# Optimization experiments

Measured on AMD Instinct MI355X. Metric: run time of the kernel, lower is better.

## Reference

```python
import jax, jax.numpy as jnp
import numpy as np

B, N, DIM = 8, 512, 512
HEADS, HD = 8, 64          # head_dim = dim // num_heads
E_ATT = 24                 # num_attn_experts, top-k = HEADS
E_FFD, K_FFD = 16, 2       # num_ffd_experts, top-k = ffd_heads
HID = 1024                 # int(dim*mlp_ratio) // ffd_heads = 2048 // 2
TASKS = 9
SWITCH_W, Z_W = 0.01, 0.001
SCALE = HD ** -0.5


def layer_norm(x, g, b, eps=1e-5):
    m = x.mean(-1, keepdims=True)
    v = ((x - m) ** 2).mean(-1, keepdims=True)
    return (x - m) * jax.lax.rsqrt(v + eps) * g + b


def top_k_gating(xf, w_gate, k, n_experts):
    # xf: [T, C], w_gate: [C, E]  (eval mode: no noise)
    logits = xf @ w_gate                                      # [T, E]
    probs = jax.nn.softmax(logits, axis=-1)
    vals, idx = jax.lax.top_k(probs, k)                       # [T, k]
    denom = jax.lax.stop_gradient(vals.sum(-1, keepdims=True) + 1e-6)
    gates = vals / denom                                      # renormalized top-k gates
    one_hot = jax.nn.one_hot(idx, n_experts, dtype=probs.dtype)  # [T, k, E]
    freqs = jax.lax.stop_gradient(one_hot.sum((0, 1)))        # tokens per expert [E]
    p_sum = probs.sum(0)
    switch = n_experts * jnp.sum((p_sum / p_sum.sum()) * (freqs / freqs.sum()))
    z = jnp.mean(jax.nn.logsumexp(logits, axis=-1) ** 2)
    loss = SWITCH_W * switch + Z_W * z
    return gates, one_hot, loss


def _forward(x, task_bh, norm1_g, norm1_b, gate_att, wq, wo_att, kv_w, kv_b,
             norm2_g, norm2_b, gate_mlp, wi, bi, wo_mlp, bo):
    Bs, Ns, C = x.shape
    T = Bs * Ns
    # ---- MoE task attention (MoA-style: experts produce query heads) ----
    x1 = layer_norm(x, norm1_g, norm1_b).reshape(T, C)
    gates, oh, loss1 = top_k_gating(x1, gate_att[task_bh], HEADS, E_ATT)
    # map: per-slot expert query projection (not gate-weighted)
    q_all = jnp.einsum('tc,ech->teh', x1, wq)                 # [T, E, hd]
    q = jnp.einsum('teh,tke->tkh', q_all, oh)                 # [T, H, hd]
    q = q.reshape(Bs, Ns, HEADS, HD)
    kv = x1 @ kv_w + kv_b                                     # shared single-head k,v
    k_, v_ = jnp.split(kv.reshape(Bs, Ns, 2 * HD), 2, axis=-1)
    attn = jnp.einsum('bihd,bjd->bhij', q, k_) * SCALE
    attn = jax.nn.softmax(attn, axis=-1)
    o = jnp.einsum('bhij,bjd->bihd', attn, v_).reshape(T, HEADS, HD)
    # reduce: gate-weighted per-expert output projection
    comb = jnp.einsum('tkd,tk,tke->ted', o, gates, oh)        # [T, E, hd]
    y = jnp.einsum('ted,edc->tc', comb, wo_att).reshape(Bs, Ns, C)
    x = x + y
    # ---- MoE task MLP ----
    x2 = layer_norm(x, norm2_g, norm2_b).reshape(T, C)
    gates2, oh2, loss2 = top_k_gating(x2, gate_mlp[task_bh], K_FFD, E_FFD)
    g_dense = jnp.einsum('tk,tke->te', gates2, oh2)           # sparse gates densified [T,E]
    h = jax.nn.gelu(jnp.einsum('tc,ech->teh', x2, wi) + bi, approximate=False)
    y2 = jnp.einsum('teh,te,ehc->tc', h, g_dense, wo_mlp) + g_dense @ bo
    x = x + y2.reshape(Bs, Ns, C)
    return x, loss1 + loss2


def setup_inputs() -> dict:
    key = jax.random.key(0)
    ks = jax.random.split(key, 8)
    s = 0.02
    return {
        'x': jax.random.normal(ks[0], (B, N, DIM), jnp.float32),
        'task_bh': 3,
        'norm1_g': jnp.ones((DIM,), jnp.float32),
        'norm1_b': jnp.zeros((DIM,), jnp.float32),
        'gate_att': jax.random.normal(ks[1], (TASKS, DIM, E_ATT), jnp.float32) * s,
        'wq': jax.random.normal(ks[2], (E_ATT, DIM, HD), jnp.float32) * s,
        'wo_att': jax.random.normal(ks[3], (E_ATT, HD, DIM), jnp.float32) * s,
        'kv_w': jax.random.normal(ks[4], (DIM, 2 * HD), jnp.float32) * s,
        'kv_b': jnp.zeros((2 * HD,), jnp.float32),
        'norm2_g': jnp.ones((DIM,), jnp.float32),
        'norm2_b': jnp.zeros((DIM,), jnp.float32),
        'gate_mlp': jax.random.normal(ks[5], (TASKS, DIM, E_FFD), jnp.float32) * s,
        'wi': jax.random.normal(ks[6], (E_FFD, DIM, HID), jnp.float32) * s,
        'bi': jnp.zeros((E_FFD, HID), jnp.float32),
        'wo_mlp': jax.random.normal(ks[7], (E_FFD, HID, DIM), jnp.float32) * s,
        'bo': jnp.zeros((E_FFD, DIM), jnp.float32),
    }


def reference(x, task_bh, norm1_g, norm1_b, gate_att, wq, wo_att, kv_w, kv_b,
              norm2_g, norm2_b, gate_mlp, wi, bi, wo_mlp, bo):
    return _forward(x, task_bh, norm1_g, norm1_b, gate_att, wq, wo_att, kv_w, kv_b,
                    norm2_g, norm2_b, gate_mlp, wi, bi, wo_mlp, bo)
```

## Files before the change

### kernel.cpp

```cpp
#include <hip/hip_runtime.h>
#include <math.h>

namespace {

constexpr int T   = 4096;
constexpr int C   = 512;
constexpr int NB  = 8;
constexpr int NS  = 512;
constexpr int HD  = 64;
constexpr int KA  = 8;
constexpr int EA  = 24;
constexpr int EF  = 16;
constexpr int KF  = 2;
constexpr int HID = 1024;

typedef __attribute__((ext_vector_type(8))) short bf16x8;
typedef __attribute__((ext_vector_type(4))) float f32x4;

__device__ inline unsigned short f2bf(float f) {
  unsigned u = __float_as_uint(f);
  return (unsigned short)((u + 0x7FFFu + ((u >> 16) & 1u)) >> 16);
}
__device__ inline float bf2f(unsigned short u) {
  return __uint_as_float((unsigned)u << 16);
}

template <int E, int TS>
__device__ inline bool tile_from_counts(const int* counts, int tile, int& e_out, int& t0_out) {
  int e = 0;
  for (; e < E; e++) {
    int nt = (counts[e] + TS - 1) / TS;
    if (tile < nt) break;
    tile -= nt;
  }
  e_out = e; t0_out = tile * TS;
  return e < E;
}

template <int E, int K>
__global__ __launch_bounds__(512) void ln_gate_kernel(
    const float* __restrict__ in, const float* __restrict__ g,
    const float* __restrict__ b, const float* __restrict__ gate_all,
    const int* __restrict__ task, unsigned short* __restrict__ outb,
    float* __restrict__ probs, float* __restrict__ lse_out,
    float* __restrict__ gates, int* __restrict__ idxs) {
  constexpr int TPB = 16;
  constexpr int XSS = 516;
  constexpr int WSS = 516;
  int tid = threadIdx.x, lane = tid & 63, wv = tid >> 6;
  int tb = blockIdx.x * TPB;
  __shared__ float xs[TPB][XSS];
  __shared__ float lg[TPB][E];
  __shared__ __align__(16) float Wt[E][WSS];
  const float* W = gate_all + (size_t)task[0] * C * E;
  for (int i = tid; i < C * E; i += 512) {
    int c = i / E, e = i - c * E;
    Wt[e][c] = W[i];
  }
  int c0 = lane * 8;
  const float4 g0 = *(const float4*)&g[c0], g1 = *(const float4*)&g[c0 + 4];
  const float4 b0 = *(const float4*)&b[c0], b1 = *(const float4*)&b[c0 + 4];
  #pragma unroll
  for (int i = 0; i < 2; i++) {
    int tt = wv * 2 + i;
    int t = tb + tt;
    const float* row = in + (size_t)t * C + c0;
    const float4 v0 = *(const float4*)&row[0];
    const float4 v1 = *(const float4*)&row[4];
    float s = (v0.x + v0.y) + (v0.z + v0.w) + (v1.x + v1.y) + (v1.z + v1.w);
    #pragma unroll
    for (int m = 1; m < 64; m <<= 1) s += __shfl_xor(s, m);
    float mean = s * (1.f / C);
    float d[8] = {v0.x - mean, v0.y - mean, v0.z - mean, v0.w - mean,
                  v1.x - mean, v1.y - mean, v1.z - mean, v1.w - mean};
    float vv = 0.f;
    #pragma unroll
    for (int j = 0; j < 8; j++) vv += d[j] * d[j];
    #pragma unroll
    for (int m = 1; m < 64; m <<= 1) vv += __shfl_xor(vv, m);
    float r = rsqrtf(vv * (1.f / C) + 1e-5f);
    float o[8];
    o[0] = d[0] * r * g0.x + b0.x; o[1] = d[1] * r * g0.y + b0.y;
    o[2] = d[2] * r * g0.z + b0.z; o[3] = d[3] * r * g0.w + b0.w;
    o[4] = d[4] * r * g1.x + b1.x; o[5] = d[5] * r * g1.y + b1.y;
    o[6] = d[6] * r * g1.z + b1.z; o[7] = d[7] * r * g1.w + b1.w;
    *(ushort4*)&outb[(size_t)t * C + c0] =
        make_ushort4(f2bf(o[0]), f2bf(o[1]), f2bf(o[2]), f2bf(o[3]));
    *(ushort4*)&outb[(size_t)t * C + c0 + 4] =
        make_ushort4(f2bf(o[4]), f2bf(o[5]), f2bf(o[6]), f2bf(o[7]));
    #pragma unroll
    for (int j = 0; j < 8; j++) xs[tt][c0 + j] = o[j];
  }
  __syncthreads();
  if (tid < TPB * E) {
    int e = tid % E, tt = tid / E;
    float a0 = 0.f, a1 = 0.f, a2 = 0.f, a3 = 0.f;
    float a4 = 0.f, a5 = 0.f, a6 = 0.f, a7 = 0.f;
    #pragma unroll 4
    for (int c = 0; c < C; c += 8) {
      const float4 xv0 = *(const float4*)&xs[tt][c];
      const float4 xv1 = *(const float4*)&xs[tt][c + 4];
      const float4 wv0 = *(const float4*)&Wt[e][c];
      const float4 wv1 = *(const float4*)&Wt[e][c + 4];
      a0 += xv0.x * wv0.x; a1 += xv0.y * wv0.y;
      a2 += xv0.z * wv0.z; a3 += xv0.w * wv0.w;
      a4 += xv1.x * wv1.x; a5 += xv1.y * wv1.y;
      a6 += xv1.z * wv1.z; a7 += xv1.w * wv1.w;
    }
    lg[tt][e] = ((a0 + a1) + (a2 + a3)) + ((a4 + a5) + (a6 + a7));
  }
  __syncthreads();
  #pragma unroll
  for (int i = 0; i < 2; i++) {
    int tt = wv * 2 + i;
    int t = tb + tt;
    float lgv = (lane < E) ? lg[tt][lane] : -3.0e38f;
    float mx = lgv;
    #pragma unroll
    for (int m = 1; m < 64; m <<= 1) mx = fmaxf(mx, __shfl_xor(mx, m));
    float pe = (lane < E) ? expf(lgv - mx) : 0.f;
    float sum = pe;
    #pragma unroll
    for (int m = 1; m < 64; m <<= 1) sum += __shfl_xor(sum, m);
    float inv = 1.f / sum;
    float prob = pe * inv;
    if (lane < E) probs[(size_t)t * E + lane] = prob;
    if (lane == 0) lse_out[t] = mx + logf(sum);
    float pv = (lane < E) ? prob : -1.f;
    float gsum = 0.f, myv = 0.f; int myi = 0;
    for (int k = 0; k < K; k++) {
      float bv = pv; int bi_ = lane;
      #pragma unroll
      for (int m = 1; m < 64; m <<= 1) {
        float ov = __shfl_xor(bv, m); int oi = __shfl_xor(bi_, m);
        if (ov > bv || (ov == bv && oi < bi_)) { bv = ov; bi_ = oi; }
      }
      gsum += bv;
      if (lane == k) { myv = bv; myi = bi_; }
      if (lane == bi_) pv = -1.f;
    }
    if (lane < K) {
      float ginv = 1.f / (gsum + 1e-6f);
      gates[(size_t)t * K + lane] = myv * ginv;
      idxs[(size_t)t * K + lane]  = myi;
    }
  }
}

template <int E>
__global__ __launch_bounds__(512) void bucket_kernel(const int* __restrict__ idx, int nslots,
                                                     int stride, int* counts, int* bucket) {
  __shared__ int lcount[E];
  __shared__ int lbase[E];
  int tid = threadIdx.x;
  if (tid < E) lcount[tid] = 0;
  __syncthreads();
  int s = blockIdx.x * 512 + tid;
  int e = 0, lpos = 0;
  bool valid = (s < nslots);
  if (valid) {
    e = idx[s];
    lpos = atomicAdd(&lcount[e], 1);
  }
  __syncthreads();
  if (tid < E) lbase[tid] = lcount[tid] ? atomicAdd(&counts[tid], lcount[tid]) : 0;
  __syncthreads();
  if (valid) bucket[(size_t)e * stride + lbase[e] + lpos] = s;
}

__global__ __launch_bounds__(256) void tcvt_all(
    const float* __restrict__ wq, const float* __restrict__ wo_a,
    const float* __restrict__ wi, const float* __restrict__ wo_m,
    const float* __restrict__ kvw,
    unsigned short* __restrict__ wqt, unsigned short* __restrict__ woat,
    unsigned short* __restrict__ wit, unsigned short* __restrict__ womt,
    unsigned short* __restrict__ kvwt) {
  int bid = blockIdx.x;
  const float* src; unsigned short* dst; int K, N, nx, rem;
  if (bid < 768)        { src = wq;   dst = wqt;  K = 512;  N = 64;   nx = 2;  rem = bid; }
  else if (bid < 1536)  { src = wo_a; dst = woat; K = 64;   N = 512;  nx = 16; rem = bid - 768; }
  else if (bid < 9728)  { src = wi;   dst = wit;  K = 512;  N = 1024; nx = 32; rem = bid - 1536; }
  else if (bid < 17920) { src = wo_m; dst = womt; K = 1024; N = 512;  nx = 16; rem = bid - 9728; }
  else                  { src = kvw;  dst = kvwt; K = 512;  N = 128;  nx = 4;  rem = bid - 17920; }
  int per = nx * (K / 32);
  int e = rem / per, r2 = rem % per;
  int kt = (r2 / nx) * 32, nt = (r2 % nx) * 32;
  __shared__ float tile[32][33];
  int tid = threadIdx.x;
  const float* S = src + (size_t)e * K * N;
  for (int i = tid; i < 32 * 32; i += 256) {
    int r = i >> 5, c = i & 31;
    tile[r][c] = S[(size_t)(kt + r) * N + nt + c];
  }
  __syncthreads();
  unsigned short* D = dst + (size_t)e * K * N;
  for (int i = tid; i < 32 * 8; i += 256) {
    int n = i >> 3, k4 = (i & 7) * 4;
    ushort4 v;
    v.x = f2bf(tile[k4 + 0][n]); v.y = f2bf(tile[k4 + 1][n]);
    v.z = f2bf(tile[k4 + 2][n]); v.w = f2bf(tile[k4 + 3][n]);
    *(ushort4*)&D[(size_t)(nt + n) * K + kt + k4] = v;
  }
}

__global__ __launch_bounds__(256) void qgemm_mfma(
    const unsigned short* __restrict__ xb, const unsigned short* __restrict__ wqt,
    const int* __restrict__ bucket, const int* __restrict__ counts,
    unsigned short* __restrict__ qb) {
  __shared__ int se, st0;
  int tid = threadIdx.x;
  if (tid == 0) {
    int e, t0;
    bool ok = tile_from_counts<EA, 64>(counts, blockIdx.y, e, t0);
    se = ok ? e : -1; st0 = t0;
  }
  __syncthreads();
  if (se < 0) return;
  int e = se, t0 = st0;
  int cnt = counts[e];
  __shared__ int slots[64];
  __shared__ __align__(16) unsigned short Xb[64][72];
  __shared__ __align__(16) unsigned short Wb[64][72];
  if (tid < 64) {
    int ii = t0 + tid;
    slots[tid] = (ii < cnt) ? bucket[(size_t)e * (T * KA) + ii] : -1;
  }
  __syncthreads();
  int lane = tid & 63, w = tid >> 6;
  int lr = lane & 15, lk = (lane >> 4) * 8, rowq = (lane >> 4) * 4;
  f32x4 acc[4] = {};
  for (int kc = 0; kc < C; kc += 64) {
    __syncthreads();
    #pragma unroll
    for (int it = 0; it < 2; ++it) {
      int i = it * 256 + tid;
      int r = i >> 3, c8 = (i & 7) * 8;
      int s = slots[r];
      uint4 v = make_uint4(0u, 0u, 0u, 0u);
      if (s >= 0) v = *(const uint4*)&xb[(size_t)(s >> 3) * C + kc + c8];
      *(uint4*)&Xb[r][c8] = v;
    }
    #pragma unroll
    for (int it = 0; it < 2; ++it) {
      int i = it * 256 + tid;
      int r = i >> 3, c8 = (i & 7) * 8;
      *(uint4*)&Wb[r][c8] = *(const uint4*)&wqt[((size_t)e * HD + r) * C + kc + c8];
    }
    __syncthreads();
    #pragma unroll
    for (int kk = 0; kk < 64; kk += 32) {
      bf16x8 a = *(const bf16x8*)&Wb[w * 16 + lr][kk + lk];
      #pragma unroll
      for (int mf = 0; mf < 4; mf++) {
        bf16x8 b = *(const bf16x8*)&Xb[mf * 16 + lr][kk + lk];
        acc[mf] = __builtin_amdgcn_mfma_f32_16x16x32_bf16(a, b, acc[mf], 0, 0, 0);
      }
    }
  }
  #pragma unroll
  for (int mf = 0; mf < 4; mf++) {
    int s = slots[mf * 16 + lr];
    if (s < 0) continue;
    ushort4 v = make_ushort4(f2bf(0.125f * acc[mf][0]), f2bf(0.125f * acc[mf][1]),
                             f2bf(0.125f * acc[mf][2]), f2bf(0.125f * acc[mf][3]));
    *(ushort4*)&qb[(size_t)s * HD + w * 16 + rowq] = v;
  }
}

__global__ __launch_bounds__(256) void kv_mfma(
    const unsigned short* __restrict__ xb, const unsigned short* __restrict__ kvwt,
    const float* __restrict__ kvb, unsigned short* __restrict__ Kb,
    unsigned short* __restrict__ Vt) {
  int t0 = blockIdx.x * 16;
  int tid = threadIdx.x;
  __shared__ __align__(16) unsigned short Xs[16][72];
  __shared__ __align__(16) unsigned short Ws[128][72];
  int lane = tid & 63, w = tid >> 6;
  int lr = lane & 15, lk = (lane >> 4) * 8, rowq = (lane >> 4) * 4;
  f32x4 acc[2] = {};
  for (int kc = 0; kc < C; kc += 64) {
    __syncthreads();
    if (tid < 128) {
      int r = tid >> 3, c8 = (tid & 7) * 8;
      *(uint4*)&Xs[r][c8] = *(const uint4*)&xb[(size_t)(t0 + r) * C + kc + c8];
    }
    #pragma unroll
    for (int it = 0; it < 4; ++it) {
      int i = it * 256 + tid;
      int r = i >> 3, c8 = (i & 7) * 8;
      *(uint4*)&Ws[r][c8] = *(const uint4*)&kvwt[(size_t)r * C + kc + c8];
    }
    __syncthreads();
    #pragma unroll
    for (int kk = 0; kk < 64; kk += 32) {
      bf16x8 xf = *(const bf16x8*)&Xs[lr][kk + lk];
      #pragma unroll
      for (int cf = 0; cf < 2; cf++) {
        bf16x8 wf = *(const bf16x8*)&Ws[w * 32 + cf * 16 + lr][kk + lk];
        acc[cf] = __builtin_amdgcn_mfma_f32_16x16x32_bf16(wf, xf, acc[cf], 0, 0, 0);
      }
    }
  }
  int t = t0 + lr;
  int bb = t >> 9, n = t & (NS - 1);
  #pragma unroll
  for (int cf = 0; cf < 2; cf++) {
    #pragma unroll
    for (int r2 = 0; r2 < 4; r2++) {
      int c = w * 32 + cf * 16 + rowq + r2;
      float v = acc[cf][r2] + kvb[c];
      if (c < HD) Kb[(size_t)t * HD + c] = f2bf(v);
      else        Vt[((size_t)bb * HD + (c - HD)) * NS + n] = f2bf(v);
    }
  }
}

__global__ __launch_bounds__(256) void attn_mfma(
    const unsigned short* __restrict__ qb, const unsigned short* __restrict__ Kb,
    const unsigned short* __restrict__ Vt, unsigned short* __restrict__ ob) {
  int qt = blockIdx.x, h = blockIdx.y, b = blockIdx.z;
  int tid = threadIdx.x;
  __shared__ __align__(16) unsigned short Qs[64][72];
  __shared__ __align__(16) unsigned short Ks[64][72];
  __shared__ __align__(16) unsigned short Vs[64][72];
  __shared__ __align__(16) unsigned short Ps[64][72];
  int i0 = qt * 64;
  #pragma unroll
  for (int it = 0; it < 2; ++it) {
    int i = it * 256 + tid;
    int r = i >> 3, c8 = (i & 7) * 8;
    *(uint4*)&Qs[r][c8] = *(const uint4*)&qb[(((size_t)(b * NS + i0 + r)) * KA + h) * HD + c8];
  }
  int lane = tid & 63, w = tid >> 6;
  int lr = lane & 15, lk = (lane >> 4) * 8, rowq = (lane >> 4) * 4;
  f32x4 acc_o[4] = {};
  float m_run = -3.0e38f, l_run = 0.f;
  for (int jt = 0; jt < NS / 64; ++jt) {
    __syncthreads();
    #pragma unroll
    for (int it = 0; it < 2; ++it) {
      int i = it * 256 + tid;
      int r = i >> 3, c8 = (i & 7) * 8;
      *(uint4*)&Ks[r][c8] = *(const uint4*)&Kb[((size_t)(b * NS + jt * 64 + r)) * HD + c8];
      *(uint4*)&Vs[r][c8] = *(const uint4*)&Vt[((size_t)b * HD + r) * NS + jt * 64 + c8];
    }
    __syncthreads();
    f32x4 acc_s[4] = {};
    #pragma unroll
    for (int kk = 0; kk < 64; kk += 32) {
      bf16x8 qf = *(const bf16x8*)&Qs[w * 16 + lr][kk + lk];
      #pragma unroll
      for (int kf = 0; kf < 4; kf++) {
        bf16x8 kr = *(const bf16x8*)&Ks[kf * 16 + lr][kk + lk];
        acc_s[kf] = __builtin_amdgcn_mfma_f32_16x16x32_bf16(kr, qf, acc_s[kf], 0, 0, 0);
      }
    }
    float pmax = acc_s[0][0];
    #pragma unroll
    for (int kf = 0; kf < 4; kf++)
      #pragma unroll
      for (int r = 0; r < 4; r++) pmax = fmaxf(pmax, acc_s[kf][r]);
    pmax = fmaxf(pmax, __shfl_xor(pmax, 16));
    pmax = fmaxf(pmax, __shfl_xor(pmax, 32));
    float m_new = fmaxf(m_run, pmax);
    float scl = expf(m_run - m_new);
    float rs = 0.f;
    #pragma unroll
    for (int kf = 0; kf < 4; kf++)
      #pragma unroll
      for (int r = 0; r < 4; r++) {
        float pv = expf(acc_s[kf][r] - m_new);
        rs += pv;
        Ps[w * 16 + lr][kf * 16 + rowq + r] = f2bf(pv);
      }
    rs += __shfl_xor(rs, 16);
    rs += __shfl_xor(rs, 32);
    l_run = l_run * scl + rs;
    m_run = m_new;
    __syncthreads();
    #pragma unroll
    for (int df = 0; df < 4; df++) {
      acc_o[df][0] *= scl; acc_o[df][1] *= scl;
      acc_o[df][2] *= scl; acc_o[df][3] *= scl;
    }
    #pragma unroll
    for (int kk = 0; kk < 64; kk += 32) {
      bf16x8 pf = *(const bf16x8*)&Ps[w * 16 + lr][kk + lk];
      #pragma unroll
      for (int df = 0; df < 4; df++) {
        bf16x8 vf = *(const bf16x8*)&Vs[df * 16 + lr][kk + lk];
        acc_o[df] = __builtin_amdgcn_mfma_f32_16x16x32_bf16(vf, pf, acc_o[df], 0, 0, 0);
      }
    }
  }
  float inv = 1.f / l_run;
  int token = b * NS + i0 + w * 16 + lr;
  #pragma unroll
  for (int df = 0; df < 4; df++) {
    ushort4 v = make_ushort4(f2bf(acc_o[df][0] * inv), f2bf(acc_o[df][1] * inv),
                             f2bf(acc_o[df][2] * inv), f2bf(acc_o[df][3] * inv));
    *(ushort4*)&ob[((size_t)token * KA + h) * HD + df * 16 + rowq] = v;
  }
}

__global__ __launch_bounds__(256) void oproj_mfma(
    const unsigned short* __restrict__ ob, const unsigned short* __restrict__ wot,
    const float* __restrict__ gates, const int* __restrict__ bucket,
    const int* __restrict__ counts, unsigned short* __restrict__ y_slot) {
  __shared__ int se, st0;
  int tid = threadIdx.x;
  if (tid == 0) {
    int e, t0;
    bool ok = tile_from_counts<EA, 128>(counts, blockIdx.y, e, t0);
    se = ok ? e : -1; st0 = t0;
  }
  __syncthreads();
  if (se < 0) return;
  int e = se, t0 = st0;
  int c0 = blockIdx.x * 128;
  int cnt = counts[e];
  __shared__ int slots[128];
  __shared__ float gs[128];
  __shared__ __align__(16) unsigned short Xb[128][72];
  __shared__ __align__(16) unsigned short Wb[128][72];
  if (tid < 128) {
    int ii = t0 + tid;
    int s = (ii < cnt) ? bucket[(size_t)e * (T * KA) + ii] : -1;
    slots[tid] = s;
    gs[tid] = (s >= 0) ? gates[s] : 0.f;
  }
  __syncthreads();
  #pragma unroll
  for (int it = 0; it < 4; ++it) {
    int i = it * 256 + tid;
    int r = i >> 3, c8 = (i & 7) * 8;
    int s = slots[r];
    uint4 vo = make_uint4(0u, 0u, 0u, 0u);
    if (s >= 0) {
      float g = gs[r];
      uint4 u = *(const uint4*)&ob[(size_t)s * HD + c8];
      const unsigned short* us = (const unsigned short*)&u;
      unsigned short* vs = (unsigned short*)&vo;
      #pragma unroll
      for (int k = 0; k < 8; k++) vs[k] = f2bf(g * bf2f(us[k]));
    }
    *(uint4*)&Xb[r][c8] = vo;
  }
  #pragma unroll
  for (int it = 0; it < 4; ++it) {
    int i = it * 256 + tid;
    int r = i >> 3, c8 = (i & 7) * 8;
    *(uint4*)&Wb[r][c8] = *(const uint4*)&wot[((size_t)e * C + c0 + r) * HD + c8];
  }
  __syncthreads();
  int lane = tid & 63, wid = tid >> 6;
  int wr = wid & 1, wc = wid >> 1;
  int lr = lane & 15, lk = (lane >> 4) * 8, rowq = (lane >> 4) * 4;
  f32x4 acc[4][4] = {};
  #pragma unroll
  for (int kk = 0; kk < 64; kk += 32) {
    bf16x8 a[4], b[4];
    #pragma unroll
    for (int nf = 0; nf < 4; nf++) a[nf] = *(const bf16x8*)&Wb[wc * 64 + nf * 16 + lr][kk + lk];
    #pragma unroll
    for (int mf = 0; mf < 4; mf++) b[mf] = *(const bf16x8*)&Xb[wr * 64 + mf * 16 + lr][kk + lk];
    #pragma unroll
    for (int nf = 0; nf < 4; nf++)
      #pragma unroll
      for (int mf = 0; mf < 4; mf++)
        acc[nf][mf] = __builtin_amdgcn_mfma_f32_16x16x32_bf16(a[nf], b[mf], acc[nf][mf], 0, 0, 0);
  }
  #pragma unroll
  for (int mf = 0; mf < 4; mf++) {
    int si = wr * 64 + mf * 16 + lr;
    int s = slots[si];
    if (s < 0) continue;
    size_t base = (size_t)s * C + c0 + wc * 64;
    #pragma unroll
    for (int nf = 0; nf < 4; nf++) {
      ushort4 v = make_ushort4(f2bf(acc[nf][mf][0]), f2bf(acc[nf][mf][1]),
                               f2bf(acc[nf][mf][2]), f2bf(acc[nf][mf][3]));
      *(ushort4*)&y_slot[base + nf * 16 + rowq] = v;
    }
  }
}

__global__ void combine_kernel(const float* __restrict__ x, const unsigned short* __restrict__ ys,
                               float* __restrict__ out) {
  int t = blockIdx.x, tid = threadIdx.x;
  int c = tid * 2;
  float s0 = 0.f, s1 = 0.f;
  #pragma unroll
  for (int k = 0; k < KA; k++) {
    unsigned u = *(const unsigned*)&ys[((size_t)t * KA + k) * C + c];
    s0 += bf2f((unsigned short)(u & 0xFFFF));
    s1 += bf2f((unsigned short)(u >> 16));
  }
  out[(size_t)t * C + c]     = x[(size_t)t * C + c] + s0;
  out[(size_t)t * C + c + 1] = x[(size_t)t * C + c + 1] + s1;
}

__global__ __launch_bounds__(256) void mlp1_mfma(
    const unsigned short* __restrict__ xb, const unsigned short* __restrict__ wit,
    const float* __restrict__ bi, const int* __restrict__ bucket,
    const int* __restrict__ counts, unsigned short* __restrict__ h) {
  __shared__ int se, st0;
  int tid = threadIdx.x;
  if (tid == 0) {
    int e, t0;
    bool ok = tile_from_counts<EF, 64>(counts, blockIdx.y, e, t0);
    se = ok ? e : -1; st0 = t0;
  }
  __syncthreads();
  if (se < 0) return;
  int e = se, t0 = st0;
  int j0 = blockIdx.x * 64;
  int cnt = counts[e];
  __shared__ int slots[64];
  __shared__ __align__(16) unsigned short Xb[64][72];
  __shared__ __align__(16) unsigned short Wb[64][72];
  if (tid < 64) {
    int ii = t0 + tid;
    slots[tid] = (ii < cnt) ? bucket[(size_t)e * (T * KF) + ii] : -1;
  }
  __syncthreads();
  int lane = tid & 63, w = tid >> 6;
  int lr = lane & 15, lk = (lane >> 4) * 8, rowq = (lane >> 4) * 4;
  f32x4 acc[4] = {};
  for (int kc = 0; kc < C; kc += 64) {
    __syncthreads();
    #pragma unroll
    for (int it = 0; it < 2; ++it) {
      int i = it * 256 + tid;
      int r = i >> 3, c8 = (i & 7) * 8;
      int s = slots[r];
      uint4 v = make_uint4(0u, 0u, 0u, 0u);
      if (s >= 0) v = *(const uint4*)&xb[(size_t)(s >> 1) * C + kc + c8];
      *(uint4*)&Xb[r][c8] = v;
    }
    #pragma unroll
    for (int it = 0; it < 2; ++it) {
      int i = it * 256 + tid;
      int r = i >> 3, c8 = (i & 7) * 8;
      *(uint4*)&Wb[r][c8] = *(const uint4*)&wit[((size_t)e * HID + j0 + r) * C + kc + c8];
    }
    __syncthreads();
    #pragma unroll
    for (int kk = 0; kk < 64; kk += 32) {
      bf16x8 a = *(const bf16x8*)&Wb[w * 16 + lr][kk + lk];
      #pragma unroll
      for (int mf = 0; mf < 4; mf++) {
        bf16x8 b = *(const bf16x8*)&Xb[mf * 16 + lr][kk + lk];
        acc[mf] = __builtin_amdgcn_mfma_f32_16x16x32_bf16(a, b, acc[mf], 0, 0, 0);
      }
    }
  }
  #pragma unroll
  for (int mf = 0; mf < 4; mf++) {
    int s = slots[mf * 16 + lr];
    if (s < 0) continue;
    int j = j0 + w * 16 + rowq;
    const float4 b4 = *(const float4*)&bi[(size_t)e * HID + j];
    float v0 = acc[mf][0] + b4.x, v1 = acc[mf][1] + b4.y;
    float v2 = acc[mf][2] + b4.z, v3 = acc[mf][3] + b4.w;
    v0 = 0.5f * v0 * (1.f + erff(v0 * 0.70710678118654752f));
    v1 = 0.5f * v1 * (1.f + erff(v1 * 0.70710678118654752f));
    v2 = 0.5f * v2 * (1.f + erff(v2 * 0.70710678118654752f));
    v3 = 0.5f * v3 * (1.f + erff(v3 * 0.70710678118654752f));
    *(ushort4*)&h[(size_t)s * HID + j] = make_ushort4(f2bf(v0), f2bf(v1), f2bf(v2), f2bf(v3));
  }
}

__global__ __launch_bounds__(256) void mlp2_mfma(
    const unsigned short* __restrict__ h, const unsigned short* __restrict__ wot,
    const float* __restrict__ bo, const float* __restrict__ gates2,
    const int* __restrict__ bucket, const int* __restrict__ counts,
    unsigned short* __restrict__ y2) {
  __shared__ int se, st0;
  int tid = threadIdx.x;
  if (tid == 0) {
    int e, t0;
    bool ok = tile_from_counts<EF, 64>(counts, blockIdx.y, e, t0);
    se = ok ? e : -1; st0 = t0;
  }
  __syncthreads();
  if (se < 0) return;
  int e = se, t0 = st0;
  int c0 = blockIdx.x * 64;
  int cnt = counts[e];
  __shared__ int slots[64];
  __shared__ __align__(16) unsigned short Xb[64][72];
  __shared__ __align__(16) unsigned short Wb[64][72];
  if (tid < 64) {
    int ii = t0 + tid;
    slots[tid] = (ii < cnt) ? bucket[(size_t)e * (T * KF) + ii] : -1;
  }
  __syncthreads();
  int lane = tid & 63, w = tid >> 6;
  int lr = lane & 15, lk = (lane >> 4) * 8, rowq = (lane >> 4) * 4;
  f32x4 acc[4] = {};
  for (int kc = 0; kc < HID; kc += 64) {
    __syncthreads();
    #pragma unroll
    for (int it = 0; it < 2; ++it) {
      int i = it * 256 + tid;
      int r = i >> 3, c8 = (i & 7) * 8;
      int s = slots[r];
      uint4 v = make_uint4(0u, 0u, 0u, 0u);
      if (s >= 0) v = *(const uint4*)&h[(size_t)s * HID + kc + c8];
      *(uint4*)&Xb[r][c8] = v;
    }
    #pragma unroll
    for (int it = 0; it < 2; ++it) {
      int i = it * 256 + tid;
      int r = i >> 3, c8 = (i & 7) * 8;
      *(uint4*)&Wb[r][c8] = *(const uint4*)&wot[((size_t)e * C + c0 + r) * HID + kc + c8];
    }
    __syncthreads();
    #pragma unroll
    for (int kk = 0; kk < 64; kk += 32) {
      bf16x8 a = *(const bf16x8*)&Wb[w * 16 + lr][kk + lk];
      #pragma unroll
      for (int mf = 0; mf < 4; mf++) {
        bf16x8 b = *(const bf16x8*)&Xb[mf * 16 + lr][kk + lk];
        acc[mf] = __builtin_amdgcn_mfma_f32_16x16x32_bf16(a, b, acc[mf], 0, 0, 0);
      }
    }
  }
  #pragma unroll
  for (int mf = 0; mf < 4; mf++) {
    int s = slots[mf * 16 + lr];
    if (s < 0) continue;
    float g = gates2[s];
    int cc = c0 + w * 16 + rowq;
    const float4 b4 = *(const float4*)&bo[(size_t)e * C + cc];
    ushort4 v = make_ushort4(f2bf(g * (acc[mf][0] + b4.x)),
                             f2bf(g * (acc[mf][1] + b4.y)),
                             f2bf(g * (acc[mf][2] + b4.z)),
                             f2bf(g * (acc[mf][3] + b4.w)));
    *(ushort4*)&y2[(size_t)s * C + cc] = v;
  }
}

__global__ void final_kernel(const unsigned short* __restrict__ y2, float* __restrict__ xout) {
  int t = blockIdx.x, tid = threadIdx.x;
  int c = tid * 2;
  unsigned u0 = *(const unsigned*)&y2[(size_t)(t * 2) * C + c];
  unsigned u1 = *(const unsigned*)&y2[(size_t)(t * 2 + 1) * C + c];
  xout[(size_t)t * C + c]     += bf2f((unsigned short)(u0 & 0xFFFF)) + bf2f((unsigned short)(u1 & 0xFFFF));
  xout[(size_t)t * C + c + 1] += bf2f((unsigned short)(u0 >> 16)) + bf2f((unsigned short)(u1 >> 16));
}

template <int E, int K, int TPB>
__global__ __launch_bounds__(256) void reduce_gating(
    const float* __restrict__ probs, const float* __restrict__ lse,
    const int* __restrict__ idxs, float* __restrict__ psum,
    float* __restrict__ freq, float* __restrict__ zsum) {
  constexpr int TPW = TPB / 4;
  int tid = threadIdx.x, lane = tid & 63, wv = tid >> 6;
  int t0 = blockIdx.x * TPB + wv * TPW;
  float ps = 0.f, fr = 0.f;
  if (lane < E) {
    for (int i = 0; i < TPW; i++) {
      int t = t0 + i;
      ps += probs[(size_t)t * E + lane];
      #pragma unroll
      for (int k = 0; k < K; k++)
        fr += (idxs[(size_t)t * K + k] == lane) ? 1.f : 0.f;
    }
  }
  float z = 0.f;
  for (int i = lane; i < TPW; i += 64) {
    float l = lse[t0 + i];
    z += l * l;
  }
  #pragma unroll
  for (int m = 1; m < 64; m <<= 1) z += __shfl_xor(z, m);
  __shared__ float sps[4][E];
  __shared__ float sfr[4][E];
  __shared__ float sz[4];
  if (lane < E) { sps[wv][lane] = ps; sfr[wv][lane] = fr; }
  if (lane == 0) sz[wv] = z;
  __syncthreads();
  if (tid < E) {
    atomicAdd(&psum[tid], sps[0][tid] + sps[1][tid] + sps[2][tid] + sps[3][tid]);
    atomicAdd(&freq[tid], sfr[0][tid] + sfr[1][tid] + sfr[2][tid] + sfr[3][tid]);
  }
  if (tid == 255) atomicAdd(zsum, sz[0] + sz[1] + sz[2] + sz[3]);
}

__global__ void loss_kernel(const float* __restrict__ acc, float* __restrict__ out) {
  const float* p1 = acc;      const float* f1 = acc + 24; float z1 = acc[48];
  const float* p2 = acc + 49; const float* f2 = acc + 65; float z2 = acc[81];
  float sp1 = 0.f, sf1 = 0.f;
  for (int e = 0; e < 24; e++) { sp1 += p1[e]; sf1 += f1[e]; }
  float sw1 = 0.f;
  for (int e = 0; e < 24; e++) sw1 += (p1[e] / sp1) * (f1[e] / sf1);
  sw1 *= 24.f;
  float sp2 = 0.f, sf2 = 0.f;
  for (int e = 0; e < 16; e++) { sp2 += p2[e]; sf2 += f2[e]; }
  float sw2 = 0.f;
  for (int e = 0; e < 16; e++) sw2 += (p2[e] / sp2) * (f2[e] / sf2);
  sw2 *= 16.f;
  out[0] = 0.01f * sw1 + 0.001f * (z1 / T) + 0.01f * sw2 + 0.001f * (z2 / T);
}

}

extern "C" void kernel_launch(void* const* d_in, const int* in_sizes, int n_in,
                              void* d_out, int out_size, void* d_ws, size_t ws_size,
                              hipStream_t stream) {
  const float* x      = (const float*)d_in[0];
  const int*   task   = (const int*)d_in[1];
  const float* n1g    = (const float*)d_in[2];
  const float* n1b    = (const float*)d_in[3];
  const float* gate_a = (const float*)d_in[4];
  const float* wq     = (const float*)d_in[5];
  const float* wo_a   = (const float*)d_in[6];
  const float* kvw    = (const float*)d_in[7];
  const float* kvb    = (const float*)d_in[8];
  const float* n2g    = (const float*)d_in[9];
  const float* n2b    = (const float*)d_in[10];
  const float* gate_m = (const float*)d_in[11];
  const float* wi     = (const float*)d_in[12];
  const float* bi     = (const float*)d_in[13];
  const float* wo_m   = (const float*)d_in[14];
  const float* bo     = (const float*)d_in[15];
  float* out = (float*)d_out;

  char* p = (char*)d_ws;
  unsigned short* x1b = (unsigned short*)p; p += (size_t)T * C * 2;
  unsigned short* qb = (unsigned short*)p;  p += (size_t)T * KA * HD * 2;
  unsigned short* ob = (unsigned short*)p;  p += (size_t)T * KA * HD * 2;
  unsigned short* Kb = (unsigned short*)p;  p += (size_t)T * HD * 2;
  unsigned short* Vt = (unsigned short*)p;  p += (size_t)T * HD * 2;
  char* un = p;                      p += (size_t)T * KA * C * 2;
  unsigned short* y_slot  = (unsigned short*)un;
  unsigned short* h       = (unsigned short*)un;
  unsigned short* y2_slot = (unsigned short*)(un + (size_t)T * KF * HID * 2);
  unsigned short* wqt = (unsigned short*)p;  p += (size_t)EA * C * HD * 2;
  unsigned short* woat = (unsigned short*)p; p += (size_t)EA * HD * C * 2;
  unsigned short* wit = (unsigned short*)p;  p += (size_t)EF * C * HID * 2;
  unsigned short* womt = (unsigned short*)p; p += (size_t)EF * HID * C * 2;
  unsigned short* kvwt = (unsigned short*)p; p += (size_t)(2 * HD) * C * 2;
  float* probs1 = (float*)p;         p += (size_t)T * EA * 4;
  float* lse1 = (float*)p;           p += (size_t)T * 4;
  float* gates1 = (float*)p;         p += (size_t)T * KA * 4;
  int* idx1 = (int*)p;               p += (size_t)T * KA * 4;
  float* probs2 = (float*)p;         p += (size_t)T * EF * 4;
  float* lse2 = (float*)p;           p += (size_t)T * 4;
  float* gates2 = (float*)p;         p += (size_t)T * KF * 4;
  int* idx2 = (int*)p;               p += (size_t)T * KF * 4;
  int* bucket_a = (int*)p;           p += (size_t)EA * (T * KA) * 4;
  int* bucket_f = (int*)p;           p += (size_t)EF * (T * KF) * 4;
  int* counts_a = (int*)p;           p += 32 * 4;
  int* counts_f = (int*)p;           p += 32 * 4;
  float* accum = (float*)p;          p += 128 * 4;

  hipMemsetAsync(counts_a, 0, (32 + 32 + 128) * 4, stream);

  tcvt_all<<<17984, 256, 0, stream>>>(wq, wo_a, wi, wo_m, kvw, wqt, woat, wit, womt, kvwt);

  ln_gate_kernel<EA, KA><<<T / 16, 512, 0, stream>>>(x, n1g, n1b, gate_a, task, x1b,
                                                     probs1, lse1, gates1, idx1);
  bucket_kernel<EA><<<(T * KA + 511) / 512, 512, 0, stream>>>(idx1, T * KA, T * KA,
                                                              counts_a, bucket_a);
  qgemm_mfma<<<dim3(1, 536), 256, 0, stream>>>(x1b, wqt, bucket_a, counts_a, qb);
  kv_mfma<<<T / 16, 256, 0, stream>>>(x1b, kvwt, kvb, Kb, Vt);
  attn_mfma<<<dim3(NS / 64, KA, NB), 256, 0, stream>>>(qb, Kb, Vt, ob);
  oproj_mfma<<<dim3(4, 280), 256, 0, stream>>>(ob, woat, gates1, bucket_a, counts_a, y_slot);
  combine_kernel<<<T, 256, 0, stream>>>(x, y_slot, out);
  ln_gate_kernel<EF, KF><<<T / 16, 512, 0, stream>>>(out, n2g, n2b, gate_m, task, x1b,
                                                     probs2, lse2, gates2, idx2);
  bucket_kernel<EF><<<(T * KF + 511) / 512, 512, 0, stream>>>(idx2, T * KF, T * KF,
                                                              counts_f, bucket_f);
  mlp1_mfma<<<dim3(16, 144), 256, 0, stream>>>(x1b, wit, bi, bucket_f, counts_f, h);
  mlp2_mfma<<<dim3(8, 144), 256, 0, stream>>>(h, womt, bo, gates2, bucket_f, counts_f, y2_slot);
  final_kernel<<<T, 256, 0, stream>>>(y2_slot, out);
  reduce_gating<EA, KA, 64><<<T / 64, 256, 0, stream>>>(probs1, lse1, idx1, accum,
                                                        accum + 24, accum + 48);
  reduce_gating<EF, KF, 64><<<T / 64, 256, 0, stream>>>(probs2, lse2, idx2, accum + 49,
                                                        accum + 65, accum + 81);
  loss_kernel<<<1, 1, 0, stream>>>(accum, out + (size_t)T * C);
}
```

Before: 233.5 us.

## Fuse residual combine into second LN-gate kernel and merge gating reductions

The separate combine kernel is removed. The second layernorm/gating kernel now sums the eight bf16 expert slot outputs into x itself and writes the residual. The LN-gate kernel moves to 1024 threads with one token per wave, and the gate dot product is split into two halves over C to use more threads. The two reduce_gating launches become one 2D launch. This saves launches and one round trip of the residual through memory, at the cost of larger blocks and more work in each LN kernel.

```diff
diff --git a/kernel.cpp b/kernel.cpp
--- a/kernel.cpp
+++ b/kernel.cpp
@@ -37,36 +37,47 @@
   return e < E;
 }
 
-template <int E, int K>
-__global__ __launch_bounds__(512) void ln_gate_kernel(
-    const float* __restrict__ in, const float* __restrict__ g,
-    const float* __restrict__ b, const float* __restrict__ gate_all,
-    const int* __restrict__ task, unsigned short* __restrict__ outb,
+template <int E, int K, bool RESID>
+__global__ __launch_bounds__(1024) void ln_gate_kernel(
+    const float* __restrict__ in, const unsigned short* __restrict__ yslot,
+    float* __restrict__ resid_out,
+    const float* __restrict__ g, const float* __restrict__ b,
+    const float* __restrict__ gate_all, const int* __restrict__ task,
+    unsigned short* __restrict__ outb,
     float* __restrict__ probs, float* __restrict__ lse_out,
     float* __restrict__ gates, int* __restrict__ idxs) {
   constexpr int TPB = 16;
   constexpr int XSS = 516;
-  constexpr int WSS = 516;
   int tid = threadIdx.x, lane = tid & 63, wv = tid >> 6;
   int tb = blockIdx.x * TPB;
   __shared__ float xs[TPB][XSS];
-  __shared__ float lg[TPB][E];
-  __shared__ __align__(16) float Wt[E][WSS];
+  __shared__ float lp[2][TPB][E];
+  __shared__ __align__(16) float Wt[E][XSS];
   const float* W = gate_all + (size_t)task[0] * C * E;
-  for (int i = tid; i < C * E; i += 512) {
+  for (int i = tid; i < C * E; i += 1024) {
     int c = i / E, e = i - c * E;
     Wt[e][c] = W[i];
   }
   int c0 = lane * 8;
   const float4 g0 = *(const float4*)&g[c0], g1 = *(const float4*)&g[c0 + 4];
   const float4 b0 = *(const float4*)&b[c0], b1 = *(const float4*)&b[c0 + 4];
-  #pragma unroll
-  for (int i = 0; i < 2; i++) {
-    int tt = wv * 2 + i;
+  {
+    int tt = wv;
     int t = tb + tt;
     const float* row = in + (size_t)t * C + c0;
-    const float4 v0 = *(const float4*)&row[0];
-    const float4 v1 = *(const float4*)&row[4];
+    float4 v0 = *(const float4*)&row[0];
+    float4 v1 = *(const float4*)&row[4];
+    if (RESID) {
+      #pragma unroll
+      for (int k = 0; k < KA; k++) {
+        uint4 u = *(const uint4*)&yslot[((size_t)t * KA + k) * C + c0];
+        const unsigned short* us = (const unsigned short*)&u;
+        v0.x += bf2f(us[0]); v0.y += bf2f(us[1]); v0.z += bf2f(us[2]); v0.w += bf2f(us[3]);
+        v1.x += bf2f(us[4]); v1.y += bf2f(us[5]); v1.z += bf2f(us[6]); v1.w += bf2f(us[7]);
+      }
+      *(float4*)&resid_out[(size_t)t * C + c0]     = v0;
+      *(float4*)&resid_out[(size_t)t * C + c0 + 4] = v1;
+    }
     float s = (v0.x + v0.y) + (v0.z + v0.w) + (v1.x + v1.y) + (v1.z + v1.w);
     #pragma unroll
     for (int m = 1; m < 64; m <<= 1) s += __shfl_xor(s, m);
@@ -92,12 +103,15 @@
     for (int j = 0; j < 8; j++) xs[tt][c0 + j] = o[j];
   }
   __syncthreads();
-  if (tid < TPB * E) {
-    int e = tid % E, tt = tid / E;
+  if (tid < TPB * E * 2) {
+    int half = tid / (TPB * E);
+    int rem = tid - half * (TPB * E);
+    int e = rem % E, tt = rem / E;
+    int cb = half * (C / 2);
     float a0 = 0.f, a1 = 0.f, a2 = 0.f, a3 = 0.f;
     float a4 = 0.f, a5 = 0.f, a6 = 0.f, a7 = 0.f;
     #pragma unroll 4
-    for (int c = 0; c < C; c += 8) {
+    for (int c = cb; c < cb + C / 2; c += 8) {
       const float4 xv0 = *(const float4*)&xs[tt][c];
       const float4 xv1 = *(const float4*)&xs[tt][c + 4];
       const float4 wv0 = *(const float4*)&Wt[e][c];
@@ -107,14 +121,13 @@
       a4 += xv1.x * wv1.x; a5 += xv1.y * wv1.y;
       a6 += xv1.z * wv1.z; a7 += xv1.w * wv1.w;
     }
-    lg[tt][e] = ((a0 + a1) + (a2 + a3)) + ((a4 + a5) + (a6 + a7));
-  }
-  __syncthreads();
-  #pragma unroll
-  for (int i = 0; i < 2; i++) {
-    int tt = wv * 2 + i;
+    lp[half][tt][e] = ((a0 + a1) + (a2 + a3)) + ((a4 + a5) + (a6 + a7));
+  }
+  __syncthreads();
+  {
+    int tt = wv;
     int t = tb + tt;
-    float lgv = (lane < E) ? lg[tt][lane] : -3.0e38f;
+    float lgv = (lane < E) ? (lp[0][tt][lane] + lp[1][tt][lane]) : -3.0e38f;
     float mx = lgv;
     #pragma unroll
     for (int m = 1; m < 64; m <<= 1) mx = fmaxf(mx, __shfl_xor(mx, m));
@@ -485,21 +498,6 @@
   }
 }
 
-__global__ void combine_kernel(const float* __restrict__ x, const unsigned short* __restrict__ ys,
-                               float* __restrict__ out) {
-  int t = blockIdx.x, tid = threadIdx.x;
-  int c = tid * 2;
-  float s0 = 0.f, s1 = 0.f;
-  #pragma unroll
-  for (int k = 0; k < KA; k++) {
-    unsigned u = *(const unsigned*)&ys[((size_t)t * KA + k) * C + c];
-    s0 += bf2f((unsigned short)(u & 0xFFFF));
-    s1 += bf2f((unsigned short)(u >> 16));
-  }
-  out[(size_t)t * C + c]     = x[(size_t)t * C + c] + s0;
-  out[(size_t)t * C + c + 1] = x[(size_t)t * C + c + 1] + s1;
-}
-
 __global__ __launch_bounds__(256) void mlp1_mfma(
     const unsigned short* __restrict__ xb, const unsigned short* __restrict__ wit,
     const float* __restrict__ bi, const int* __restrict__ bucket,
@@ -651,12 +649,21 @@
   xout[(size_t)t * C + c + 1] += bf2f((unsigned short)(u0 >> 16)) + bf2f((unsigned short)(u1 >> 16));
 }
 
-template <int E, int K, int TPB>
-__global__ __launch_bounds__(256) void reduce_gating(
-    const float* __restrict__ probs, const float* __restrict__ lse,
-    const int* __restrict__ idxs, float* __restrict__ psum,
-    float* __restrict__ freq, float* __restrict__ zsum) {
-  constexpr int TPW = TPB / 4;
+__global__ __launch_bounds__(256) void reduce_gating_all(
+    const float* __restrict__ probs1, const float* __restrict__ lse1,
+    const int* __restrict__ idx1,
+    const float* __restrict__ probs2, const float* __restrict__ lse2,
+    const int* __restrict__ idx2, float* __restrict__ accum) {
+  constexpr int TPB = 64, TPW = 16;
+  int which = blockIdx.y;
+  int E = which ? EF : EA;
+  int K = which ? KF : KA;
+  const float* probs = which ? probs2 : probs1;
+  const float* lse   = which ? lse2 : lse1;
+  const int* idxs    = which ? idx2 : idx1;
+  float* psum = accum + (which ? 49 : 0);
+  float* freq = accum + (which ? 65 : 24);
+  float* zsum = accum + (which ? 81 : 48);
   int tid = threadIdx.x, lane = tid & 63, wv = tid >> 6;
   int t0 = blockIdx.x * TPB + wv * TPW;
   float ps = 0.f, fr = 0.f;
@@ -664,7 +671,6 @@
     for (int i = 0; i < TPW; i++) {
       int t = t0 + i;
       ps += probs[(size_t)t * E + lane];
-      #pragma unroll
       for (int k = 0; k < K; k++)
         fr += (idxs[(size_t)t * K + k] == lane) ? 1.f : 0.f;
     }
@@ -676,8 +682,8 @@
   }
   #pragma unroll
   for (int m = 1; m < 64; m <<= 1) z += __shfl_xor(z, m);
-  __shared__ float sps[4][E];
-  __shared__ float sfr[4][E];
+  __shared__ float sps[4][EA];
+  __shared__ float sfr[4][EA];
   __shared__ float sz[4];
   if (lane < E) { sps[wv][lane] = ps; sfr[wv][lane] = fr; }
   if (lane == 0) sz[wv] = z;
@@ -761,25 +767,22 @@
 
   tcvt_all<<<17984, 256, 0, stream>>>(wq, wo_a, wi, wo_m, kvw, wqt, woat, wit, womt, kvwt);
 
-  ln_gate_kernel<EA, KA><<<T / 16, 512, 0, stream>>>(x, n1g, n1b, gate_a, task, x1b,
-                                                     probs1, lse1, gates1, idx1);
+  ln_gate_kernel<EA, KA, false><<<T / 16, 1024, 0, stream>>>(
+      x, y_slot, out, n1g, n1b, gate_a, task, x1b, probs1, lse1, gates1, idx1);
   bucket_kernel<EA><<<(T * KA + 511) / 512, 512, 0, stream>>>(idx1, T * KA, T * KA,
                                                               counts_a, bucket_a);
   qgemm_mfma<<<dim3(1, 536), 256, 0, stream>>>(x1b, wqt, bucket_a, counts_a, qb);
   kv_mfma<<<T / 16, 256, 0, stream>>>(x1b, kvwt, kvb, Kb, Vt);
   attn_mfma<<<dim3(NS / 64, KA, NB), 256, 0, stream>>>(qb, Kb, Vt, ob);
   oproj_mfma<<<dim3(4, 280), 256, 0, stream>>>(ob, woat, gates1, bucket_a, counts_a, y_slot);
-  combine_kernel<<<T, 256, 0, stream>>>(x, y_slot, out);
-  ln_gate_kernel<EF, KF><<<T / 16, 512, 0, stream>>>(out, n2g, n2b, gate_m, task, x1b,
-                                                     probs2, lse2, gates2, idx2);
+  ln_gate_kernel<EF, KF, true><<<T / 16, 1024, 0, stream>>>(
+      x, y_slot, out, n2g, n2b, gate_m, task, x1b, probs2, lse2, gates2, idx2);
   bucket_kernel<EF><<<(T * KF + 511) / 512, 512, 0, stream>>>(idx2, T * KF, T * KF,
                                                               counts_f, bucket_f);
   mlp1_mfma<<<dim3(16, 144), 256, 0, stream>>>(x1b, wit, bi, bucket_f, counts_f, h);
   mlp2_mfma<<<dim3(8, 144), 256, 0, stream>>>(h, womt, bo, gates2, bucket_f, counts_f, y2_slot);
   final_kernel<<<T, 256, 0, stream>>>(y2_slot, out);
-  reduce_gating<EA, KA, 64><<<T / 64, 256, 0, stream>>>(probs1, lse1, idx1, accum,
-                                                        accum + 24, accum + 48);
-  reduce_gating<EF, KF, 64><<<T / 64, 256, 0, stream>>>(probs2, lse2, idx2, accum + 49,
-                                                        accum + 65, accum + 81);
+  reduce_gating_all<<<dim3(T / 64, 2), 256, 0, stream>>>(probs1, lse1, idx1,
+                                                         probs2, lse2, idx2, accum);
   loss_kernel<<<1, 1, 0, stream>>>(accum, out + (size_t)T * C);
 }
```

Result: no change. 229.4 us (-1.7%).
